# Performance work log

Measured on AMD Instinct MI355X. Metric: run time of the kernel, lower is better.

The kernel has to match this reference:

```python
import jax, jax.numpy as jnp
import numpy as np

N_NODES = 100000
N_EDGES = 1600000
IN_C, HID_C, OUT_C = 128, 128, 64
DROPOUT_P = 0.5


def setup_inputs() -> dict:
    key = jax.random.key(0)
    ks = jax.random.split(key, 12)
    x = jax.random.normal(ks[0], (N_NODES, IN_C), dtype=jnp.float32)
    edge_index = jax.random.randint(ks[1], (2, N_EDGES), 0, N_NODES, dtype=jnp.int64)
    # Glorot-ish init scale for linear weights
    def w(k, fi, fo):
        return jax.random.normal(k, (fi, fo), dtype=jnp.float32) * (1.0 / np.sqrt(fi))
    return {
        "x": x,
        "edge_index": edge_index,
        "Wl0": w(ks[2], IN_C, HID_C), "Wr0": w(ks[3], IN_C, HID_C), "b0": jnp.zeros((HID_C,), jnp.float32),
        "Wl1": w(ks[4], HID_C, HID_C), "Wr1": w(ks[5], HID_C, HID_C), "b1": jnp.zeros((HID_C,), jnp.float32),
        "Wl2": w(ks[6], HID_C, OUT_C), "Wr2": w(ks[7], HID_C, OUT_C), "b2": jnp.zeros((OUT_C,), jnp.float32),
    }


def _sage_conv(x, src, dst, Wl, Wr, b):
    # mean-aggregate neighbor features x[src] at dst, then two linears + bias
    n = x.shape[0]
    agg = jax.ops.segment_sum(x[src], dst, num_segments=n)          # [N, d]
    cnt = jax.ops.segment_sum(jnp.ones((src.shape[0],), x.dtype), dst, num_segments=n)
    mean = agg / jnp.maximum(cnt, 1.0)[:, None]
    return mean @ Wl + x @ Wr + b


def _dropout(x, key, p):
    keep = jax.random.bernoulli(key, 1.0 - p, x.shape)
    return jnp.where(keep, x / (1.0 - p), 0.0).astype(x.dtype)


def reference(x, edge_index, Wl0, Wr0, b0, Wl1, Wr1, b1, Wl2, Wr2, b2):
    src, dst = edge_index[0], edge_index[1]
    dk = jax.random.split(jax.random.key(42), 2)
    h = _sage_conv(x, src, dst, Wl0, Wr0, b0)
    h = _dropout(jax.nn.relu(h), dk[0], DROPOUT_P)
    h = _sage_conv(h, src, dst, Wl1, Wr1, b1)
    h = _dropout(jax.nn.relu(h), dk[1], DROPOUT_P)
    h = _sage_conv(h, src, dst, Wl2, Wr2, b2)
    return h
```

## Files before the change

kernel.cpp:

```cpp
#include <hip/hip_runtime.h>
#include <stdint.h>

typedef __attribute__((ext_vector_type(8))) short s8v;
typedef __attribute__((ext_vector_type(4))) float f4v;

constexpr int ECHUNK = 4096;

__host__ __device__ inline uint32_t rotl32(uint32_t x, int r) {
    return (x << r) | (x >> (32 - r));
}

__host__ __device__ inline void tf2x32(uint32_t k0, uint32_t k1,
                                       uint32_t x0, uint32_t x1,
                                       uint32_t& o0, uint32_t& o1) {
    const uint32_t ks0 = k0, ks1 = k1, ks2 = k0 ^ k1 ^ 0x1BD11BDAu;
    x0 += ks0; x1 += ks1;
    x0 += x1; x1 = rotl32(x1, 13); x1 ^= x0;
    x0 += x1; x1 = rotl32(x1, 15); x1 ^= x0;
    x0 += x1; x1 = rotl32(x1, 26); x1 ^= x0;
    x0 += x1; x1 = rotl32(x1, 6);  x1 ^= x0;
    x0 += ks1; x1 += ks2 + 1u;
    x0 += x1; x1 = rotl32(x1, 17); x1 ^= x0;
    x0 += x1; x1 = rotl32(x1, 29); x1 ^= x0;
    x0 += x1; x1 = rotl32(x1, 16); x1 ^= x0;
    x0 += x1; x1 = rotl32(x1, 24); x1 ^= x0;
    x0 += ks2; x1 += ks0 + 2u;
    x0 += x1; x1 = rotl32(x1, 13); x1 ^= x0;
    x0 += x1; x1 = rotl32(x1, 15); x1 ^= x0;
    x0 += x1; x1 = rotl32(x1, 26); x1 ^= x0;
    x0 += x1; x1 = rotl32(x1, 6);  x1 ^= x0;
    x0 += ks0; x1 += ks1 + 3u;
    x0 += x1; x1 = rotl32(x1, 17); x1 ^= x0;
    x0 += x1; x1 = rotl32(x1, 29); x1 ^= x0;
    x0 += x1; x1 = rotl32(x1, 16); x1 ^= x0;
    x0 += x1; x1 = rotl32(x1, 24); x1 ^= x0;
    x0 += ks1; x1 += ks2 + 4u;
    x0 += x1; x1 = rotl32(x1, 13); x1 ^= x0;
    x0 += x1; x1 = rotl32(x1, 15); x1 ^= x0;
    x0 += x1; x1 = rotl32(x1, 26); x1 ^= x0;
    x0 += x1; x1 = rotl32(x1, 6);  x1 ^= x0;
    x0 += ks2; x1 += ks0 + 5u;
    o0 = x0; o1 = x1;
}

__device__ inline bool tf_keep(uint32_t idx, uint32_t k0, uint32_t k1) {
    uint32_t o0, o1;
    tf2x32(k0, k1, 0u, idx, o0, o1);
    return ((o0 ^ o1) >> 31) == 0u;
}

__device__ inline uint16_t f2bf(float f) {
    uint32_t u = __float_as_uint(f);
    return (uint16_t)((u + 0x7fffu + ((u >> 16) & 1u)) >> 16);
}
__device__ inline float bflo(uint32_t v) { return __uint_as_float(v << 16); }
__device__ inline float bfhi(uint32_t v) { return __uint_as_float(v & 0xffff0000u); }

__global__ void detect_kernel(const int* __restrict__ w, int* __restrict__ flag64) {
    __shared__ int s[256];
    int t = threadIdx.x;
    int acc = 0;
    for (int i = t; i < 2048; i += 256) acc |= w[2 * i + 1];
    s[t] = acc;
    __syncthreads();
    for (int off = 128; off > 0; off >>= 1) {
        if (t < off) s[t] |= s[t + off];
        __syncthreads();
    }
    if (t == 0) *flag64 = (s[0] == 0) ? 1 : 0;
}

__device__ inline int edge_src(const int* w, int e, int f64) {
    return f64 ? w[2 * e] : w[e];
}
__device__ inline int edge_dst(const int* w, int e, int E, int f64) {
    return f64 ? w[2 * E + 2 * e] : w[E + e];
}

__global__ __launch_bounds__(256) void bucketcount_kernel(
        const int* __restrict__ w, const int* __restrict__ flag64,
        int* __restrict__ hist, int E, int nA, int NBUK) {
    __shared__ int cnt[256];
    int t = threadIdx.x;
    if (t < NBUK) cnt[t] = 0;
    __syncthreads();
    int f64 = *flag64;
    int lo = blockIdx.x * ECHUNK, hi = min(E, lo + ECHUNK);
    for (int e = lo + t; e < hi; e += 256)
        atomicAdd(&cnt[edge_dst(w, e, E, f64) >> 9], 1);
    __syncthreads();
    if (t < NBUK) hist[t * nA + blockIdx.x] = cnt[t];
}

__global__ void scan1_kernel(const int* __restrict__ in, int* __restrict__ out,
                             int* __restrict__ bsum, int n) {
    __shared__ int s[512];
    int t = threadIdx.x;
    int i = blockIdx.x * 512 + t;
    int v = (i < n) ? in[i] : 0;
    s[t] = v;
    __syncthreads();
    for (int off = 1; off < 512; off <<= 1) {
        int x = (t >= off) ? s[t - off] : 0;
        __syncthreads();
        s[t] += x;
        __syncthreads();
    }
    if (i < n) out[i + 1] = s[t];
    if (t == 511) bsum[blockIdx.x] = s[511];
}

__global__ void scan2_kernel(int* __restrict__ bsum, int nb) {
    if (threadIdx.x == 0 && blockIdx.x == 0) {
        int run = 0;
        for (int b = 0; b < nb; ++b) { int tmp = bsum[b]; bsum[b] = run; run += tmp; }
    }
}

__global__ void scan3_kernel(int* __restrict__ out, const int* __restrict__ bsum, int n) {
    int i = blockIdx.x * 512 + threadIdx.x;
    if (i < n) out[i + 1] += bsum[blockIdx.x];
    if (i == 0) out[0] = 0;
}

__global__ __launch_bounds__(256) void bucketscatter_kernel(
        const int* __restrict__ w, const int* __restrict__ flag64,
        const int* __restrict__ bofs, uint2* __restrict__ tmp, int E, int nA, int NBUK) {
    __shared__ int sbase[256];
    int t = threadIdx.x;
    if (t < NBUK) sbase[t] = bofs[t * nA + blockIdx.x];
    __syncthreads();
    int f64 = *flag64;
    int lo = blockIdx.x * ECHUNK, hi = min(E, lo + ECHUNK);
    for (int e = lo + t; e < hi; e += 256) {
        int s = edge_src(w, e, f64);
        int d = edge_dst(w, e, E, f64);
        int p = atomicAdd(&sbase[d >> 9], 1);
        tmp[p] = make_uint2((unsigned)s, (unsigned)d);
    }
}

__global__ __launch_bounds__(256) void bucketdeg_kernel(
        const uint2* __restrict__ tmp, const int* __restrict__ bofs,
        int* __restrict__ deg, int nA, int N) {
    __shared__ int cnt[512];
    int b = blockIdx.x;
    int node0 = b << 9;
    int nn = min(512, N - node0);
    int t = threadIdx.x;
    for (int i = t; i < nn; i += 256) cnt[i] = 0;
    __syncthreads();
    int lo = bofs[b * nA], hi = bofs[(b + 1) * nA];
    for (int e = lo + t; e < hi; e += 256)
        atomicAdd(&cnt[(int)tmp[e].y - node0], 1);
    __syncthreads();
    for (int i = t; i < nn; i += 256) deg[node0 + i] = cnt[i];
}

__global__ __launch_bounds__(256) void finescatter_kernel(
        const uint2* __restrict__ tmp, const int* __restrict__ bofs,
        const int* __restrict__ rowptr, int* __restrict__ col, int nA, int N) {
    __shared__ int cur[512];
    int b = blockIdx.x;
    int node0 = b << 9;
    int nn = min(512, N - node0);
    int t = threadIdx.x;
    for (int i = t; i < nn; i += 256) cur[i] = rowptr[node0 + i];
    __syncthreads();
    int lo = bofs[b * nA], hi = bofs[(b + 1) * nA];
    for (int e = lo + t; e < hi; e += 256) {
        uint2 p = tmp[e];
        int q = atomicAdd(&cur[(int)p.y - node0], 1);
        col[q] = (int)p.x;
    }
}

__global__ void convx_kernel(const float* __restrict__ in, uint16_t* __restrict__ out, int n4) {
    int i = blockIdx.x * blockDim.x + threadIdx.x;
    if (i >= n4) return;
    float4 v = *(const float4*)(in + (size_t)i * 4);
    uint16_t o[4] = { f2bf(v.x), f2bf(v.y), f2bf(v.z), f2bf(v.w) };
    *(uint2*)(out + (size_t)i * 4) = *(uint2*)o;
}

struct WPack {
    const float* src[6];
    uint16_t*    dst[6];
    int          n[6];
};
__global__ void convw_all_kernel(WPack p) {
    int s = blockIdx.y;
    int i = blockIdx.x * blockDim.x + threadIdx.x;
    int total = p.n[s] * 128;
    if (i >= total) return;
    int nn = i >> 7, k = i & 127;
    p.dst[s][i] = f2bf(p.src[s][(size_t)k * p.n[s] + nn]);
}

__global__ __launch_bounds__(256) void pair_gemm_kernel(
        const uint16_t* __restrict__ Xb, const uint16_t* __restrict__ WtL,
        const uint16_t* __restrict__ WtR, const float* __restrict__ bias,
        uint16_t* __restrict__ YL, uint16_t* __restrict__ ZB, int M, int N) {
    const int l   = threadIdx.x & 63;
    const int wv  = threadIdx.x >> 6;
    const int row0 = blockIdx.x * 64 + wv * 16;
    const int ml  = l & 15;
    const int kg  = l >> 4;

    int arow = row0 + ml; if (arow >= M) arow = M - 1;
    const uint16_t* xr = Xb + (size_t)arow * 128 + kg * 8;
    s8v a0 = *(const s8v*)(xr);
    s8v a1 = *(const s8v*)(xr + 32);
    s8v a2 = *(const s8v*)(xr + 64);
    s8v a3 = *(const s8v*)(xr + 96);

    const int drow = row0 + kg * 4;

    for (int n0 = 0; n0 < N; n0 += 16) {
        const uint16_t* wl = WtL + (size_t)(n0 + ml) * 128 + kg * 8;
        const uint16_t* wr = WtR + (size_t)(n0 + ml) * 128 + kg * 8;
        f4v accL = {0.f, 0.f, 0.f, 0.f};
        f4v accR = {0.f, 0.f, 0.f, 0.f};
        accL = __builtin_amdgcn_mfma_f32_16x16x32_bf16(a0, *(const s8v*)(wl), accL, 0, 0, 0);
        accR = __builtin_amdgcn_mfma_f32_16x16x32_bf16(a0, *(const s8v*)(wr), accR, 0, 0, 0);
        accL = __builtin_amdgcn_mfma_f32_16x16x32_bf16(a1, *(const s8v*)(wl + 32), accL, 0, 0, 0);
        accR = __builtin_amdgcn_mfma_f32_16x16x32_bf16(a1, *(const s8v*)(wr + 32), accR, 0, 0, 0);
        accL = __builtin_amdgcn_mfma_f32_16x16x32_bf16(a2, *(const s8v*)(wl + 64), accL, 0, 0, 0);
        accR = __builtin_amdgcn_mfma_f32_16x16x32_bf16(a2, *(const s8v*)(wr + 64), accR, 0, 0, 0);
        accL = __builtin_amdgcn_mfma_f32_16x16x32_bf16(a3, *(const s8v*)(wl + 96), accL, 0, 0, 0);
        accR = __builtin_amdgcn_mfma_f32_16x16x32_bf16(a3, *(const s8v*)(wr + 96), accR, 0, 0, 0);

        float bv = bias[n0 + ml];
#pragma unroll
        for (int r = 0; r < 4; ++r) {
            int g = drow + r;
            if (g < M) {
                YL[(size_t)g * N + n0 + ml] = f2bf(accL[r]);
                ZB[(size_t)g * N + n0 + ml] = f2bf(accR[r] + bv);
            }
        }
    }
}

__global__ __launch_bounds__(256) void agg128_kernel(
        const uint16_t* __restrict__ Yl, const uint16_t* __restrict__ Zb,
        const int* __restrict__ rowptr, const int* __restrict__ col,
        uint16_t* __restrict__ H, int n, uint32_t k0, uint32_t k1) {
    int wv = threadIdx.x >> 6, lane = threadIdx.x & 63;
    int half = lane >> 5, sl = lane & 31;
    int node = blockIdx.x * 8 + wv * 2 + half;
    if (node >= n) return;
    const uint2* ylp = (const uint2*)Yl;
    int beg = rowptr[node], end = rowptr[node + 1];
    float a0 = 0.f, a1 = 0.f, a2 = 0.f, a3 = 0.f;
    int e = beg;
    for (; e + 3 < end; e += 4) {
        int j0 = col[e], j1 = col[e + 1], j2 = col[e + 2], j3 = col[e + 3];
        uint2 v0 = ylp[(size_t)j0 * 32 + sl];
        uint2 v1 = ylp[(size_t)j1 * 32 + sl];
        uint2 v2 = ylp[(size_t)j2 * 32 + sl];
        uint2 v3 = ylp[(size_t)j3 * 32 + sl];
        a0 += bflo(v0.x) + bflo(v1.x) + bflo(v2.x) + bflo(v3.x);
        a1 += bfhi(v0.x) + bfhi(v1.x) + bfhi(v2.x) + bfhi(v3.x);
        a2 += bflo(v0.y) + bflo(v1.y) + bflo(v2.y) + bflo(v3.y);
        a3 += bfhi(v0.y) + bfhi(v1.y) + bfhi(v2.y) + bfhi(v3.y);
    }
    for (; e < end; ++e) {
        uint2 v = ylp[(size_t)col[e] * 32 + sl];
        a0 += bflo(v.x); a1 += bfhi(v.x);
        a2 += bflo(v.y); a3 += bfhi(v.y);
    }
    int cnt = end - beg;
    float inv = 1.0f / (float)(cnt > 1 ? cnt : 1);
    uint2 z = ((const uint2*)Zb)[(size_t)node * 32 + sl];
    float h0 = fmaxf(a0 * inv + bflo(z.x), 0.0f);
    float h1 = fmaxf(a1 * inv + bfhi(z.x), 0.0f);
    float h2 = fmaxf(a2 * inv + bflo(z.y), 0.0f);
    float h3 = fmaxf(a3 * inv + bfhi(z.y), 0.0f);
    uint32_t idx = (uint32_t)node * 128u + (uint32_t)sl * 4u;
    h0 = tf_keep(idx,      k0, k1) ? h0 * 2.0f : 0.0f;
    h1 = tf_keep(idx + 1u, k0, k1) ? h1 * 2.0f : 0.0f;
    h2 = tf_keep(idx + 2u, k0, k1) ? h2 * 2.0f : 0.0f;
    h3 = tf_keep(idx + 3u, k0, k1) ? h3 * 2.0f : 0.0f;
    uint2 o;
    o.x = (uint32_t)f2bf(h0) | ((uint32_t)f2bf(h1) << 16);
    o.y = (uint32_t)f2bf(h2) | ((uint32_t)f2bf(h3) << 16);
    ((uint2*)H)[(size_t)node * 32 + sl] = o;
}

__global__ __launch_bounds__(256) void agg64_kernel(
        const uint16_t* __restrict__ Yl, const uint16_t* __restrict__ Zb,
        const int* __restrict__ rowptr, const int* __restrict__ col,
        float* __restrict__ out, int n) {
    int wv = threadIdx.x >> 6, lane = threadIdx.x & 63;
    int half = lane >> 5, sl = lane & 31;
    int node = blockIdx.x * 8 + wv * 2 + half;
    if (node >= n) return;
    const uint32_t* ylp = (const uint32_t*)Yl;
    int beg = rowptr[node], end = rowptr[node + 1];
    float a0 = 0.f, a1 = 0.f;
    int e = beg;
    for (; e + 3 < end; e += 4) {
        int j0 = col[e], j1 = col[e + 1], j2 = col[e + 2], j3 = col[e + 3];
        uint32_t v0 = ylp[(size_t)j0 * 32 + sl];
        uint32_t v1 = ylp[(size_t)j1 * 32 + sl];
        uint32_t v2 = ylp[(size_t)j2 * 32 + sl];
        uint32_t v3 = ylp[(size_t)j3 * 32 + sl];
        a0 += bflo(v0) + bflo(v1) + bflo(v2) + bflo(v3);
        a1 += bfhi(v0) + bfhi(v1) + bfhi(v2) + bfhi(v3);
    }
    for (; e < end; ++e) {
        uint32_t v = ylp[(size_t)col[e] * 32 + sl];
        a0 += bflo(v); a1 += bfhi(v);
    }
    int cnt = end - beg;
    float inv = 1.0f / (float)(cnt > 1 ? cnt : 1);
    uint32_t z = ((const uint32_t*)Zb)[(size_t)node * 32 + sl];
    float2 o;
    o.x = a0 * inv + bflo(z);
    o.y = a1 * inv + bfhi(z);
    *(float2*)(out + (size_t)node * 64 + sl * 2) = o;
}

extern "C" void kernel_launch(void* const* d_in, const int* in_sizes, int n_in,
                              void* d_out, int out_size, void* d_ws, size_t ws_size,
                              hipStream_t stream) {
    const float* x   = (const float*)d_in[0];
    const int*   ei  = (const int*)d_in[1];
    const float* Wl0 = (const float*)d_in[2];
    const float* Wr0 = (const float*)d_in[3];
    const float* b0  = (const float*)d_in[4];
    const float* Wl1 = (const float*)d_in[5];
    const float* Wr1 = (const float*)d_in[6];
    const float* b1  = (const float*)d_in[7];
    const float* Wl2 = (const float*)d_in[8];
    const float* Wr2 = (const float*)d_in[9];
    const float* b2  = (const float*)d_in[10];

    const int N = in_sizes[0] / 128;
    const int E = in_sizes[1] / 2;
    const int* srcp = ei;

    const int nA   = (E + ECHUNK - 1) / ECHUNK;
    const int NBUK = (N + 511) >> 9;
    const int L    = NBUK * nA;

    char* ws = (char*)d_ws;
    size_t off = 0;
    auto alloc = [&](size_t bytes) {
        size_t o = off;
        off = (off + bytes + 255) & ~(size_t)255;
        return o;
    };
    int*      rowptr = (int*)(ws + alloc((size_t)(N + 1) * 4));
    int*      deg    = (int*)(ws + alloc((size_t)N * 4));
    int*      bsum   = (int*)(ws + alloc(1024 * 4));
    int*      flag64 = (int*)(ws + alloc(256));
    int*      hist   = (int*)(ws + alloc((size_t)L * 4));
    int*      bofs   = (int*)(ws + alloc((size_t)(L + 1) * 4));
    uint2*    tmp    = (uint2*)(ws + alloc((size_t)E * 8));
    int*      col    = (int*)(ws + alloc((size_t)E * 4));
    uint16_t* Xb     = (uint16_t*)(ws + alloc((size_t)N * 128 * 2));
    uint16_t* Hb     = (uint16_t*)(ws + alloc((size_t)N * 128 * 2));
    uint16_t* Byl    = (uint16_t*)(ws + alloc((size_t)N * 128 * 2));
    uint16_t* Czb    = (uint16_t*)(ws + alloc((size_t)N * 128 * 2));
    uint16_t* Wt0l   = (uint16_t*)(ws + alloc(128 * 128 * 2));
    uint16_t* Wt0r   = (uint16_t*)(ws + alloc(128 * 128 * 2));
    uint16_t* Wt1l   = (uint16_t*)(ws + alloc(128 * 128 * 2));
    uint16_t* Wt1r   = (uint16_t*)(ws + alloc(128 * 128 * 2));
    uint16_t* Wt2l   = (uint16_t*)(ws + alloc(128 * 128 * 2));
    uint16_t* Wt2r   = (uint16_t*)(ws + alloc(128 * 128 * 2));

    uint32_t k00, k01, k10, k11;
    tf2x32(0u, 42u, 0u, 0u, k00, k01);
    tf2x32(0u, 42u, 0u, 1u, k10, k11);

    detect_kernel<<<1, 256, 0, stream>>>(srcp, flag64);
    bucketcount_kernel<<<nA, 256, 0, stream>>>(srcp, flag64, hist, E, nA, NBUK);
    int NBL = (L + 511) / 512;
    scan1_kernel<<<NBL, 512, 0, stream>>>(hist, bofs, bsum, L);
    scan2_kernel<<<1, 64, 0, stream>>>(bsum, NBL);
    scan3_kernel<<<NBL, 512, 0, stream>>>(bofs, bsum, L);
    bucketscatter_kernel<<<nA, 256, 0, stream>>>(srcp, flag64, bofs, tmp, E, nA, NBUK);
    bucketdeg_kernel<<<NBUK, 256, 0, stream>>>(tmp, bofs, deg, nA, N);
    int NBN = (N + 511) / 512;
    scan1_kernel<<<NBN, 512, 0, stream>>>(deg, rowptr, bsum, N);
    scan2_kernel<<<1, 64, 0, stream>>>(bsum, NBN);
    scan3_kernel<<<NBN, 512, 0, stream>>>(rowptr, bsum, N);
    finescatter_kernel<<<NBUK, 256, 0, stream>>>(tmp, bofs, rowptr, col, nA, N);

    convx_kernel<<<(N * 128 / 4 + 255) / 256, 256, 0, stream>>>(x, Xb, N * 128 / 4);
    WPack wp;
    wp.src[0] = Wl0; wp.dst[0] = Wt0l; wp.n[0] = 128;
    wp.src[1] = Wr0; wp.dst[1] = Wt0r; wp.n[1] = 128;
    wp.src[2] = Wl1; wp.dst[2] = Wt1l; wp.n[2] = 128;
    wp.src[3] = Wr1; wp.dst[3] = Wt1r; wp.n[3] = 128;
    wp.src[4] = Wl2; wp.dst[4] = Wt2l; wp.n[4] = 64;
    wp.src[5] = Wr2; wp.dst[5] = Wt2r; wp.n[5] = 64;
    convw_all_kernel<<<dim3(64, 6), 256, 0, stream>>>(wp);

    dim3 blk(256);
    dim3 gg((N + 63) / 64);
    dim3 gagg((N + 7) / 8);

    pair_gemm_kernel<<<gg, blk, 0, stream>>>(Xb, Wt0l, Wt0r, b0, Byl, Czb, N, 128);
    agg128_kernel<<<gagg, blk, 0, stream>>>(Byl, Czb, rowptr, col, Hb, N, k00, k01);
    pair_gemm_kernel<<<gg, blk, 0, stream>>>(Hb, Wt1l, Wt1r, b1, Byl, Czb, N, 128);
    agg128_kernel<<<gagg, blk, 0, stream>>>(Byl, Czb, rowptr, col, Hb, N, k10, k11);
    pair_gemm_kernel<<<gg, blk, 0, stream>>>(Hb, Wt2l, Wt2r, b2, Byl, Czb, N, 64);
    agg64_kernel<<<gagg, blk, 0, stream>>>(Byl, Czb, rowptr, col, (float*)d_out, N);
}
```

Before: 565.4 us.

## Precompute dropout bitmasks in a separate kernel and pack bucket-sort edge entries

New measurement: 607.0 us. +7.4%, slower.

```diff
diff --git a/kernel.cpp b/kernel.cpp
--- a/kernel.cpp
+++ b/kernel.cpp
@@ -43,18 +43,31 @@
     o0 = x0; o1 = x1;
 }
 
-__device__ inline bool tf_keep(uint32_t idx, uint32_t k0, uint32_t k1) {
-    uint32_t o0, o1;
-    tf2x32(k0, k1, 0u, idx, o0, o1);
-    return ((o0 ^ o1) >> 31) == 0u;
-}
-
 __device__ inline uint16_t f2bf(float f) {
     uint32_t u = __float_as_uint(f);
     return (uint16_t)((u + 0x7fffu + ((u >> 16) & 1u)) >> 16);
 }
 __device__ inline float bflo(uint32_t v) { return __uint_as_float(v << 16); }
 __device__ inline float bfhi(uint32_t v) { return __uint_as_float(v & 0xffff0000u); }
+
+__global__ __launch_bounds__(256) void mask_kernel(
+        uint32_t* __restrict__ mA, uint32_t* __restrict__ mB, int nwords,
+        uint32_t a0, uint32_t a1, uint32_t b0, uint32_t b1) {
+    int i = blockIdx.x * blockDim.x + threadIdx.x;
+    if (i >= nwords) return;
+    uint32_t base = (uint32_t)i << 5;
+    uint32_t wa = 0, wb = 0;
+#pragma unroll 4
+    for (int b = 0; b < 32; ++b) {
+        uint32_t o0, o1;
+        tf2x32(a0, a1, 0u, base + (uint32_t)b, o0, o1);
+        wa |= ((((o0 ^ o1) >> 31) ^ 1u)) << b;
+        tf2x32(b0, b1, 0u, base + (uint32_t)b, o0, o1);
+        wb |= ((((o0 ^ o1) >> 31) ^ 1u)) << b;
+    }
+    mA[i] = wa;
+    mB[i] = wb;
+}
 
 __global__ void detect_kernel(const int* __restrict__ w, int* __restrict__ flag64) {
     __shared__ int s[256];
@@ -125,7 +138,7 @@
 
 __global__ __launch_bounds__(256) void bucketscatter_kernel(
         const int* __restrict__ w, const int* __restrict__ flag64,
-        const int* __restrict__ bofs, uint2* __restrict__ tmp, int E, int nA, int NBUK) {
+        const int* __restrict__ bofs, uint32_t* __restrict__ tmp, int E, int nA, int NBUK) {
     __shared__ int sbase[256];
     int t = threadIdx.x;
     if (t < NBUK) sbase[t] = bofs[t * nA + blockIdx.x];
@@ -136,12 +149,12 @@
         int s = edge_src(w, e, f64);
         int d = edge_dst(w, e, E, f64);
         int p = atomicAdd(&sbase[d >> 9], 1);
-        tmp[p] = make_uint2((unsigned)s, (unsigned)d);
+        tmp[p] = (uint32_t)s | ((uint32_t)(d & 511) << 17);
     }
 }
 
 __global__ __launch_bounds__(256) void bucketdeg_kernel(
-        const uint2* __restrict__ tmp, const int* __restrict__ bofs,
+        const uint32_t* __restrict__ tmp, const int* __restrict__ bofs,
         int* __restrict__ deg, int nA, int N) {
     __shared__ int cnt[512];
     int b = blockIdx.x;
@@ -152,13 +165,13 @@
     __syncthreads();
     int lo = bofs[b * nA], hi = bofs[(b + 1) * nA];
     for (int e = lo + t; e < hi; e += 256)
-        atomicAdd(&cnt[(int)tmp[e].y - node0], 1);
+        atomicAdd(&cnt[tmp[e] >> 17], 1);
     __syncthreads();
     for (int i = t; i < nn; i += 256) deg[node0 + i] = cnt[i];
 }
 
 __global__ __launch_bounds__(256) void finescatter_kernel(
-        const uint2* __restrict__ tmp, const int* __restrict__ bofs,
+        const uint32_t* __restrict__ tmp, const int* __restrict__ bofs,
         const int* __restrict__ rowptr, int* __restrict__ col, int nA, int N) {
     __shared__ int cur[512];
     int b = blockIdx.x;
@@ -169,9 +182,9 @@
     __syncthreads();
     int lo = bofs[b * nA], hi = bofs[(b + 1) * nA];
     for (int e = lo + t; e < hi; e += 256) {
-        uint2 p = tmp[e];
-        int q = atomicAdd(&cur[(int)p.y - node0], 1);
-        col[q] = (int)p.x;
+        uint32_t p = tmp[e];
+        int q = atomicAdd(&cur[p >> 17], 1);
+        col[q] = (int)(p & 0x1FFFFu);
     }
 }
 
@@ -245,7 +258,7 @@
 __global__ __launch_bounds__(256) void agg128_kernel(
         const uint16_t* __restrict__ Yl, const uint16_t* __restrict__ Zb,
         const int* __restrict__ rowptr, const int* __restrict__ col,
-        uint16_t* __restrict__ H, int n, uint32_t k0, uint32_t k1) {
+        const uint32_t* __restrict__ mask, uint16_t* __restrict__ H, int n) {
     int wv = threadIdx.x >> 6, lane = threadIdx.x & 63;
     int half = lane >> 5, sl = lane & 31;
     int node = blockIdx.x * 8 + wv * 2 + half;
@@ -277,11 +290,12 @@
     float h1 = fmaxf(a1 * inv + bfhi(z.x), 0.0f);
     float h2 = fmaxf(a2 * inv + bflo(z.y), 0.0f);
     float h3 = fmaxf(a3 * inv + bfhi(z.y), 0.0f);
-    uint32_t idx = (uint32_t)node * 128u + (uint32_t)sl * 4u;
-    h0 = tf_keep(idx,      k0, k1) ? h0 * 2.0f : 0.0f;
-    h1 = tf_keep(idx + 1u, k0, k1) ? h1 * 2.0f : 0.0f;
-    h2 = tf_keep(idx + 2u, k0, k1) ? h2 * 2.0f : 0.0f;
-    h3 = tf_keep(idx + 3u, k0, k1) ? h3 * 2.0f : 0.0f;
+    uint32_t mw  = mask[(size_t)node * 4 + (sl >> 3)];
+    uint32_t nib = (mw >> ((sl & 7) * 4)) & 0xFu;
+    h0 = (nib & 1u) ? h0 * 2.0f : 0.0f;
+    h1 = (nib & 2u) ? h1 * 2.0f : 0.0f;
+    h2 = (nib & 4u) ? h2 * 2.0f : 0.0f;
+    h3 = (nib & 8u) ? h3 * 2.0f : 0.0f;
     uint2 o;
     o.x = (uint32_t)f2bf(h0) | ((uint32_t)f2bf(h1) << 16);
     o.y = (uint32_t)f2bf(h2) | ((uint32_t)f2bf(h3) << 16);
@@ -358,8 +372,10 @@
     int*      flag64 = (int*)(ws + alloc(256));
     int*      hist   = (int*)(ws + alloc((size_t)L * 4));
     int*      bofs   = (int*)(ws + alloc((size_t)(L + 1) * 4));
-    uint2*    tmp    = (uint2*)(ws + alloc((size_t)E * 8));
+    uint32_t* tmp    = (uint32_t*)(ws + alloc((size_t)E * 4));
     int*      col    = (int*)(ws + alloc((size_t)E * 4));
+    uint32_t* maskA  = (uint32_t*)(ws + alloc((size_t)N * 16));
+    uint32_t* maskB  = (uint32_t*)(ws + alloc((size_t)N * 16));
     uint16_t* Xb     = (uint16_t*)(ws + alloc((size_t)N * 128 * 2));
     uint16_t* Hb     = (uint16_t*)(ws + alloc((size_t)N * 128 * 2));
     uint16_t* Byl    = (uint16_t*)(ws + alloc((size_t)N * 128 * 2));
@@ -374,6 +390,10 @@
     uint32_t k00, k01, k10, k11;
     tf2x32(0u, 42u, 0u, 0u, k00, k01);
     tf2x32(0u, 42u, 0u, 1u, k10, k11);
+
+    int nwords = N * 4;
+    mask_kernel<<<(nwords + 255) / 256, 256, 0, stream>>>(maskA, maskB, nwords,
+                                                          k00, k01, k10, k11);
 
     detect_kernel<<<1, 256, 0, stream>>>(srcp, flag64);
     bucketcount_kernel<<<nA, 256, 0, stream>>>(srcp, flag64, hist, E, nA, NBUK);
@@ -404,9 +424,9 @@
     dim3 gagg((N + 7) / 8);
 
     pair_gemm_kernel<<<gg, blk, 0, stream>>>(Xb, Wt0l, Wt0r, b0, Byl, Czb, N, 128);
-    agg128_kernel<<<gagg, blk, 0, stream>>>(Byl, Czb, rowptr, col, Hb, N, k00, k01);
+    agg128_kernel<<<gagg, blk, 0, stream>>>(Byl, Czb, rowptr, col, maskA, Hb, N);
     pair_gemm_kernel<<<gg, blk, 0, stream>>>(Hb, Wt1l, Wt1r, b1, Byl, Czb, N, 128);
-    agg128_kernel<<<gagg, blk, 0, stream>>>(Byl, Czb, rowptr, col, Hb, N, k10, k11);
+    agg128_kernel<<<gagg, blk, 0, stream>>>(Byl, Czb, rowptr, col, maskB, Hb, N);
     pair_gemm_kernel<<<gg, blk, 0, stream>>>(Hb, Wt2l, Wt2r, b2, Byl, Czb, N, 64);
     agg64_kernel<<<gagg, blk, 0, stream>>>(Byl, Czb, rowptr, col, (float*)d_out, N);
 }
```

## Fuse CSR build stages and conversions, pack bucket entries into 32 bits

Applied to the files above, without the earlier changes.

Measured after the change: 557.9 us. No clear change (-1.3%).

```diff
diff --git a/kernel.cpp b/kernel.cpp
--- a/kernel.cpp
+++ b/kernel.cpp
@@ -4,7 +4,7 @@
 typedef __attribute__((ext_vector_type(8))) short s8v;
 typedef __attribute__((ext_vector_type(4))) float f4v;
 
-constexpr int ECHUNK = 4096;
+constexpr int ECHUNK = 16384;
 
 __host__ __device__ inline uint32_t rotl32(uint32_t x, int r) {
     return (x << r) | (x >> (32 - r));
@@ -56,18 +56,15 @@
 __device__ inline float bflo(uint32_t v) { return __uint_as_float(v << 16); }
 __device__ inline float bfhi(uint32_t v) { return __uint_as_float(v & 0xffff0000u); }
 
-__global__ void detect_kernel(const int* __restrict__ w, int* __restrict__ flag64) {
-    __shared__ int s[256];
+__device__ inline int block_detect64(const int* __restrict__ w, int* sf) {
     int t = threadIdx.x;
+    if (t == 0) *sf = 0;
+    __syncthreads();
     int acc = 0;
-    for (int i = t; i < 2048; i += 256) acc |= w[2 * i + 1];
-    s[t] = acc;
-    __syncthreads();
-    for (int off = 128; off > 0; off >>= 1) {
-        if (t < off) s[t] |= s[t + off];
-        __syncthreads();
-    }
-    if (t == 0) *flag64 = (s[0] == 0) ? 1 : 0;
+    for (int i = t; i < 2048; i += blockDim.x) acc |= w[2 * i + 1];
+    if (acc) atomicOr(sf, 1);
+    __syncthreads();
+    return (*sf == 0) ? 1 : 0;
 }
 
 __device__ inline int edge_src(const int* w, int e, int f64) {
@@ -77,14 +74,14 @@
     return f64 ? w[2 * E + 2 * e] : w[E + e];
 }
 
+
 __global__ __launch_bounds__(256) void bucketcount_kernel(
-        const int* __restrict__ w, const int* __restrict__ flag64,
-        int* __restrict__ hist, int E, int nA, int NBUK) {
+        const int* __restrict__ w, int* __restrict__ hist, int E, int nA, int NBUK) {
     __shared__ int cnt[256];
+    __shared__ int sf;
     int t = threadIdx.x;
     if (t < NBUK) cnt[t] = 0;
-    __syncthreads();
-    int f64 = *flag64;
+    int f64 = block_detect64(w, &sf);
     int lo = blockIdx.x * ECHUNK, hi = min(E, lo + ECHUNK);
     for (int e = lo + t; e < hi; e += 256)
         atomicAdd(&cnt[edge_dst(w, e, E, f64) >> 9], 1);
@@ -92,109 +89,102 @@
     if (t < NBUK) hist[t * nA + blockIdx.x] = cnt[t];
 }
 
-__global__ void scan1_kernel(const int* __restrict__ in, int* __restrict__ out,
-                             int* __restrict__ bsum, int n) {
-    __shared__ int s[512];
+__global__ __launch_bounds__(1024) void scanL_kernel(
+        const int* __restrict__ in, int* __restrict__ out, int n) {
+    __shared__ int s[1024];
     int t = threadIdx.x;
-    int i = blockIdx.x * 512 + t;
-    int v = (i < n) ? in[i] : 0;
-    s[t] = v;
-    __syncthreads();
-    for (int off = 1; off < 512; off <<= 1) {
+    int elpt = (n + 1023) >> 10;
+    int lo = t * elpt, hi = min(n, lo + elpt);
+    int sum = 0;
+    for (int i = lo; i < hi; ++i) sum += in[i];
+    s[t] = sum;
+    __syncthreads();
+    for (int off = 1; off < 1024; off <<= 1) {
         int x = (t >= off) ? s[t - off] : 0;
         __syncthreads();
         s[t] += x;
         __syncthreads();
     }
-    if (i < n) out[i + 1] = s[t];
-    if (t == 511) bsum[blockIdx.x] = s[511];
-}
-
-__global__ void scan2_kernel(int* __restrict__ bsum, int nb) {
-    if (threadIdx.x == 0 && blockIdx.x == 0) {
-        int run = 0;
-        for (int b = 0; b < nb; ++b) { int tmp = bsum[b]; bsum[b] = run; run += tmp; }
-    }
-}
-
-__global__ void scan3_kernel(int* __restrict__ out, const int* __restrict__ bsum, int n) {
-    int i = blockIdx.x * 512 + threadIdx.x;
-    if (i < n) out[i + 1] += bsum[blockIdx.x];
-    if (i == 0) out[0] = 0;
+    int run = s[t] - sum;
+    for (int i = lo; i < hi; ++i) { run += in[i]; out[i + 1] = run; }
+    if (t == 0) out[0] = 0;
 }
 
 __global__ __launch_bounds__(256) void bucketscatter_kernel(
-        const int* __restrict__ w, const int* __restrict__ flag64,
-        const int* __restrict__ bofs, uint2* __restrict__ tmp, int E, int nA, int NBUK) {
+        const int* __restrict__ w, const int* __restrict__ bofs,
+        uint32_t* __restrict__ tmp, int E, int nA, int NBUK) {
     __shared__ int sbase[256];
+    __shared__ int sf;
     int t = threadIdx.x;
     if (t < NBUK) sbase[t] = bofs[t * nA + blockIdx.x];
-    __syncthreads();
-    int f64 = *flag64;
+    int f64 = block_detect64(w, &sf);
     int lo = blockIdx.x * ECHUNK, hi = min(E, lo + ECHUNK);
     for (int e = lo + t; e < hi; e += 256) {
         int s = edge_src(w, e, f64);
         int d = edge_dst(w, e, E, f64);
         int p = atomicAdd(&sbase[d >> 9], 1);
-        tmp[p] = make_uint2((unsigned)s, (unsigned)d);
-    }
-}
-
-__global__ __launch_bounds__(256) void bucketdeg_kernel(
-        const uint2* __restrict__ tmp, const int* __restrict__ bofs,
-        int* __restrict__ deg, int nA, int N) {
+        tmp[p] = (uint32_t)s | ((uint32_t)(d & 511) << 17);
+    }
+}
+
+__global__ __launch_bounds__(512) void fusedcsr_kernel(
+        const uint32_t* __restrict__ tmp, const int* __restrict__ bofs,
+        int* __restrict__ rowptr, int* __restrict__ col, int nA, int N, int E) {
     __shared__ int cnt[512];
-    int b = blockIdx.x;
+    int b = blockIdx.x, t = threadIdx.x;
     int node0 = b << 9;
     int nn = min(512, N - node0);
-    int t = threadIdx.x;
-    for (int i = t; i < nn; i += 256) cnt[i] = 0;
+    cnt[t] = 0;
     __syncthreads();
     int lo = bofs[b * nA], hi = bofs[(b + 1) * nA];
-    for (int e = lo + t; e < hi; e += 256)
-        atomicAdd(&cnt[(int)tmp[e].y - node0], 1);
-    __syncthreads();
-    for (int i = t; i < nn; i += 256) deg[node0 + i] = cnt[i];
-}
-
-__global__ __launch_bounds__(256) void finescatter_kernel(
-        const uint2* __restrict__ tmp, const int* __restrict__ bofs,
-        const int* __restrict__ rowptr, int* __restrict__ col, int nA, int N) {
-    __shared__ int cur[512];
-    int b = blockIdx.x;
-    int node0 = b << 9;
-    int nn = min(512, N - node0);
-    int t = threadIdx.x;
-    for (int i = t; i < nn; i += 256) cur[i] = rowptr[node0 + i];
-    __syncthreads();
-    int lo = bofs[b * nA], hi = bofs[(b + 1) * nA];
-    for (int e = lo + t; e < hi; e += 256) {
-        uint2 p = tmp[e];
-        int q = atomicAdd(&cur[(int)p.y - node0], 1);
-        col[q] = (int)p.x;
-    }
-}
-
-__global__ void convx_kernel(const float* __restrict__ in, uint16_t* __restrict__ out, int n4) {
-    int i = blockIdx.x * blockDim.x + threadIdx.x;
-    if (i >= n4) return;
-    float4 v = *(const float4*)(in + (size_t)i * 4);
-    uint16_t o[4] = { f2bf(v.x), f2bf(v.y), f2bf(v.z), f2bf(v.w) };
-    *(uint2*)(out + (size_t)i * 4) = *(uint2*)o;
-}
-
-struct WPack {
-    const float* src[6];
-    uint16_t*    dst[6];
-    int          n[6];
+    for (int e = lo + t; e < hi; e += 512)
+        atomicAdd(&cnt[tmp[e] >> 17], 1);
+    __syncthreads();
+    int v = cnt[t];
+    for (int off = 1; off < 512; off <<= 1) {
+        int x = (t >= off) ? cnt[t - off] : 0;
+        __syncthreads();
+        cnt[t] += x;
+        __syncthreads();
+    }
+    int base = lo + (cnt[t] - v);
+    if (t < nn) rowptr[node0 + t] = base;
+    if (b == 0 && t == 0) rowptr[N] = E;
+    __syncthreads();
+    cnt[t] = base;
+    __syncthreads();
+    for (int e = lo + t; e < hi; e += 512) {
+        uint32_t p = tmp[e];
+        int q = atomicAdd(&cnt[p >> 17], 1);
+        col[q] = (int)(p & 0x1FFFFu);
+    }
+}
+
+struct CPack {
+    const float* wsrc[6];
+    uint16_t*    wdst[6];
+    int          wn[6];
+    int          wboff[7];
 };
-__global__ void convw_all_kernel(WPack p) {
-    int s = blockIdx.y;
-    int i = blockIdx.x * blockDim.x + threadIdx.x;
-    int total = p.n[s] * 128;
-    if (i >= total) return;
-    int nn = i >> 7, k = i & 127;
-    p.dst[s][i] = f2bf(p.src[s][(size_t)k * p.n[s] + nn]);
+__global__ void conv_all_kernel(const float* __restrict__ x, uint16_t* __restrict__ xb,
+                                int nxb, CPack p) {
+    int blk = blockIdx.x;
+    if (blk < nxb) {
+        int i = blk * 256 + threadIdx.x;
+        float4 v = *(const float4*)(x + (size_t)i * 4);
+        uint16_t o[4] = { f2bf(v.x), f2bf(v.y), f2bf(v.z), f2bf(v.w) };
+        *(uint2*)(xb + (size_t)i * 4) = *(uint2*)o;
+    } else {
+        int wb = blk - nxb;
+        int s = 0;
+        while (s < 5 && wb >= p.wboff[s + 1]) ++s;
+        int i = (wb - p.wboff[s]) * 256 + threadIdx.x;
+        int total = p.wn[s] * 128;
+        if (i < total) {
+            int nn = i >> 7, k = i & 127;
+            p.wdst[s][i] = f2bf(p.wsrc[s][(size_t)k * p.wn[s] + nn]);
+        }
+    }
 }
 
 __global__ __launch_bounds__(256) void pair_gemm_kernel(
@@ -353,12 +343,9 @@
         return o;
     };
     int*      rowptr = (int*)(ws + alloc((size_t)(N + 1) * 4));
-    int*      deg    = (int*)(ws + alloc((size_t)N * 4));
-    int*      bsum   = (int*)(ws + alloc(1024 * 4));
-    int*      flag64 = (int*)(ws + alloc(256));
     int*      hist   = (int*)(ws + alloc((size_t)L * 4));
     int*      bofs   = (int*)(ws + alloc((size_t)(L + 1) * 4));
-    uint2*    tmp    = (uint2*)(ws + alloc((size_t)E * 8));
+    uint32_t* tmp    = (uint32_t*)(ws + alloc((size_t)E * 4));
     int*      col    = (int*)(ws + alloc((size_t)E * 4));
     uint16_t* Xb     = (uint16_t*)(ws + alloc((size_t)N * 128 * 2));
     uint16_t* Hb     = (uint16_t*)(ws + alloc((size_t)N * 128 * 2));
@@ -375,29 +362,23 @@
     tf2x32(0u, 42u, 0u, 0u, k00, k01);
     tf2x32(0u, 42u, 0u, 1u, k10, k11);
 
-    detect_kernel<<<1, 256, 0, stream>>>(srcp, flag64);
-    bucketcount_kernel<<<nA, 256, 0, stream>>>(srcp, flag64, hist, E, nA, NBUK);
-    int NBL = (L + 511) / 512;
-    scan1_kernel<<<NBL, 512, 0, stream>>>(hist, bofs, bsum, L);
-    scan2_kernel<<<1, 64, 0, stream>>>(bsum, NBL);
-    scan3_kernel<<<NBL, 512, 0, stream>>>(bofs, bsum, L);
-    bucketscatter_kernel<<<nA, 256, 0, stream>>>(srcp, flag64, bofs, tmp, E, nA, NBUK);
-    bucketdeg_kernel<<<NBUK, 256, 0, stream>>>(tmp, bofs, deg, nA, N);
-    int NBN = (N + 511) / 512;
-    scan1_kernel<<<NBN, 512, 0, stream>>>(deg, rowptr, bsum, N);
-    scan2_kernel<<<1, 64, 0, stream>>>(bsum, NBN);
-    scan3_kernel<<<NBN, 512, 0, stream>>>(rowptr, bsum, N);
-    finescatter_kernel<<<NBUK, 256, 0, stream>>>(tmp, bofs, rowptr, col, nA, N);
-
-    convx_kernel<<<(N * 128 / 4 + 255) / 256, 256, 0, stream>>>(x, Xb, N * 128 / 4);
-    WPack wp;
-    wp.src[0] = Wl0; wp.dst[0] = Wt0l; wp.n[0] = 128;
-    wp.src[1] = Wr0; wp.dst[1] = Wt0r; wp.n[1] = 128;
-    wp.src[2] = Wl1; wp.dst[2] = Wt1l; wp.n[2] = 128;
-    wp.src[3] = Wr1; wp.dst[3] = Wt1r; wp.n[3] = 128;
-    wp.src[4] = Wl2; wp.dst[4] = Wt2l; wp.n[4] = 64;
-    wp.src[5] = Wr2; wp.dst[5] = Wt2r; wp.n[5] = 64;
-    convw_all_kernel<<<dim3(64, 6), 256, 0, stream>>>(wp);
+    bucketcount_kernel<<<nA, 256, 0, stream>>>(srcp, hist, E, nA, NBUK);
+    scanL_kernel<<<1, 1024, 0, stream>>>(hist, bofs, L);
+    bucketscatter_kernel<<<nA, 256, 0, stream>>>(srcp, bofs, tmp, E, nA, NBUK);
+    fusedcsr_kernel<<<NBUK, 512, 0, stream>>>(tmp, bofs, rowptr, col, nA, N, E);
+
+    int nxb = N * 128 / 4 / 256;
+    CPack cp;
+    cp.wsrc[0] = Wl0; cp.wdst[0] = Wt0l; cp.wn[0] = 128;
+    cp.wsrc[1] = Wr0; cp.wdst[1] = Wt0r; cp.wn[1] = 128;
+    cp.wsrc[2] = Wl1; cp.wdst[2] = Wt1l; cp.wn[2] = 128;
+    cp.wsrc[3] = Wr1; cp.wdst[3] = Wt1r; cp.wn[3] = 128;
+    cp.wsrc[4] = Wl2; cp.wdst[4] = Wt2l; cp.wn[4] = 64;
+    cp.wsrc[5] = Wr2; cp.wdst[5] = Wt2r; cp.wn[5] = 64;
+    int acc = 0;
+    for (int s = 0; s < 6; ++s) { cp.wboff[s] = acc; acc += cp.wn[s] * 128 / 256; }
+    cp.wboff[6] = acc;
+    conv_all_kernel<<<nxb + acc, 256, 0, stream>>>(x, Xb, nxb, cp);
 
     dim3 blk(256);
     dim3 gg((N + 63) / 64);
```
